# Optimization experiments

Hardware: AMD Instinct MI355X
Metric: run time of the kernel (lower is better)

## Reference

```python
import jax, jax.numpy as jnp
import numpy as np

K = 1024  # codebook size
D = 256   # embedding dim


def setup_inputs() -> dict:
    key = jax.random.key(0)
    k1, k2 = jax.random.split(key)
    z_e_x = jax.random.normal(k1, (32, D, 32, 32), dtype=jnp.float32)  # NCHW
    # nn.Embedding weight initialized uniform(-1/K, 1/K)
    W = jax.random.uniform(k2, (K, D), dtype=jnp.float32, minval=-1.0 / K, maxval=1.0 / K)
    return {"z_e_x": z_e_x, "W": W}


def reference(z_e_x, W):
    # permute NCHW -> NHWC, flatten spatial, nearest-codebook lookup (vq)
    z = jnp.transpose(z_e_x, (0, 2, 3, 1))            # [B, H, Wd, D]
    B, H, Wd, Dd = z.shape
    flat = z.reshape(-1, Dd)                           # [N, D]
    # squared L2 distances: ||z||^2 - 2 z.W^T + ||W||^2
    z_sq = jnp.sum(flat * flat, axis=1, keepdims=True)         # [N, 1]
    w_sq = jnp.sum(W * W, axis=1)                               # [K]
    dists = z_sq - 2.0 * (flat @ W.T) + w_sq[None, :]           # [N, K]
    idx = jnp.argmin(dists, axis=1)                             # [N]
    latents = idx.reshape(B, H, Wd)                             # [B, H, Wd] int indices
    return latents
```

## Files before the change

### kernel.cpp

```cpp
#include <hip/hip_runtime.h>

#define NPOS 32768
#define DDIM 256
#define KCODES 1024

typedef __attribute__((ext_vector_type(8))) short bf16x8;
typedef __attribute__((ext_vector_type(4))) float f32x4;
typedef unsigned long long u64;

__device__ __forceinline__ float sqr_rn(float x) {
    float r = x * x;
    asm volatile("" : "+v"(r));
    return r;
}
__device__ __forceinline__ float add_rn(float a, float b) {
    float r = a + b;
    asm volatile("" : "+v"(r));
    return r;
}

__device__ __forceinline__ unsigned short f2bf(float x) {
    unsigned u = __float_as_uint(x);
    return (unsigned short)((u + 0x7fffu + ((u >> 16) & 1u)) >> 16);
}

__device__ __forceinline__ u64 packm(float s, int code) {
    unsigned b = __float_as_uint(s);
    unsigned mm = ((unsigned)((int)b >> 31)) | 0x80000000u;
    return ((u64)(b ^ mm) << 32) | (unsigned)code;
}

__global__ __launch_bounds__(256) void prep(const float* __restrict__ z,
                                            const float* __restrict__ W,
                                            float* __restrict__ wsq,
                                            unsigned short* __restrict__ zb16t,
                                            unsigned short* __restrict__ wb16t) {
    __shared__ unsigned short Ls[8 * 1024];
    const int t = threadIdx.x;
    if (blockIdx.x < 1024) {
        const int img = blockIdx.x >> 5;
        const int dc  = blockIdx.x & 31;
        const int kk  = dc >> 2, kq = dc & 3;
        const float* zr = z + img * (DDIM * 1024) + dc * 8 * 1024;
#pragma unroll
        for (int e = 0; e < 8; ++e) {
            const float4 v = *(const float4*)&zr[e * 1024 + t * 4];
            unsigned short* o = &Ls[e * 1024 + t * 4];
            o[0] = f2bf(v.x); o[1] = f2bf(v.y); o[2] = f2bf(v.z); o[3] = f2bf(v.w);
        }
        __syncthreads();
#pragma unroll
        for (int j = 0; j < 4; ++j) {
            const int m = t + j * 256;
            const int mtile = img * 8 + (m >> 7);
            bf16x8 o;
#pragma unroll
            for (int e = 0; e < 8; ++e) o[e] = (short)Ls[e * 1024 + m];
            *(bf16x8*)&zb16t[mtile * 32768 + kk * 4096 + kq * 1024 + (m & 127) * 8] = o;
        }
    } else {
        const int bid = blockIdx.x - 1024;
        const int row = bid * 16 + (t >> 4);
        const int j   = t & 15;
        const float* base = W + row * DDIM + (j & 7) + (j >> 3) * 128;
        float r = sqr_rn(base[0]);
#pragma unroll
        for (int i = 1; i < 16; ++i) r = add_rn(r, sqr_rn(base[i * 8]));
#pragma unroll
        for (int m = 1; m <= 8; m <<= 1) r = add_rn(r, __shfl_xor(r, m));
        if (j == 0) wsq[row] = r;
#pragma unroll
        for (int jj = 0; jj < 2; ++jj) {
            const int u  = t + jj * 256;
            const int n  = bid * 16 + (u >> 5);
            const int k8 = u & 31;
            const float4 f0 = *(const float4*)&W[n * DDIM + k8 * 8];
            const float4 f1 = *(const float4*)&W[n * DDIM + k8 * 8 + 4];
            bf16x8 o;
            o[0] = (short)f2bf(f0.x); o[1] = (short)f2bf(f0.y);
            o[2] = (short)f2bf(f0.z); o[3] = (short)f2bf(f0.w);
            o[4] = (short)f2bf(f1.x); o[5] = (short)f2bf(f1.y);
            o[6] = (short)f2bf(f1.z); o[7] = (short)f2bf(f1.w);
            const int kk = k8 >> 2, kq = k8 & 3;
            *(bf16x8*)&wb16t[(n >> 8) * 65536 + kk * 8192 + kq * 2048 + (n & 255) * 8] = o;
        }
    }
}

__global__ __launch_bounds__(256) __attribute__((amdgpu_waves_per_eu(2, 2)))
void gemm_top2(const unsigned short* __restrict__ zb16t,
               const unsigned short* __restrict__ wb16t,
               const float* __restrict__ wsq, u64* __restrict__ cand) {
    __shared__ u64 redU[4096];

    const int t    = threadIdx.x;
    const int w    = t >> 6;
    const int l    = t & 63;
    const int ln   = l & 15;
    const int q    = l >> 4;
    const int mw   = (w & 1) * 64;
    const int nw   = (w >> 1) * 128;
    const int mblk = blockIdx.x >> 2;
    const int nblk = blockIdx.x & 3;
    const int m0   = mblk * 128;
    const int n0   = nblk * 256;

    const char* aLane = (const char*)zb16t + (size_t)mblk * 65536 + q * 2048 + (mw + ln) * 16;
    const char* bLane = (const char*)wb16t + (size_t)nblk * 131072 + q * 4096 + (nw + ln) * 16;

    f32x4 acc[4][8];
#pragma unroll
    for (int a = 0; a < 4; ++a)
#pragma unroll
        for (int b = 0; b < 8; ++b) acc[a][b] = (f32x4)(0.f);

    bf16x8 afr[4], anx[4];
#pragma unroll
    for (int mf = 0; mf < 4; ++mf)
        afr[mf] = *(const bf16x8*)(aLane + mf * 256);

#pragma unroll 1
    for (int kk = 0; kk < 8; ++kk) {
        bf16x8 bfr[8];
#pragma unroll
        for (int nf = 0; nf < 8; ++nf)
            bfr[nf] = *(const bf16x8*)(bLane + kk * 16384 + nf * 256);
        if (kk < 7) {
#pragma unroll
            for (int mf = 0; mf < 4; ++mf)
                anx[mf] = *(const bf16x8*)(aLane + (kk + 1) * 8192 + mf * 256);
        }
#pragma unroll
        for (int nf = 0; nf < 8; ++nf)
#pragma unroll
            for (int mf = 0; mf < 4; ++mf)
                acc[mf][nf] = __builtin_amdgcn_mfma_f32_16x16x32_bf16(
                    afr[mf], bfr[nf], acc[mf][nf], 0, 0, 0);
#pragma unroll
        for (int mf = 0; mf < 4; ++mf) afr[mf] = anx[mf];
    }

    float wq[8];
#pragma unroll
    for (int nf = 0; nf < 8; ++nf) wq[nf] = wsq[n0 + nw + nf * 16 + ln];

#pragma unroll
    for (int mf = 0; mf < 4; ++mf) {
#pragma unroll
        for (int reg = 0; reg < 4; ++reg) {
            const int row = mw + mf * 16 + q * 4 + reg;
            float s0 = 1e30f, s1 = 1e30f;
            int   i0 = 0,     i1 = 0;
#pragma unroll
            for (int nf = 0; nf < 8; ++nf) {
                const float s  = fmaf(-2.f, acc[mf][nf][reg], wq[nf]);
                const int   cc = n0 + nw + nf * 16 + ln;
                if (s < s0)      { s1 = s0; i1 = i0; s0 = s; i0 = cc; }
                else if (s < s1) { s1 = s; i1 = cc; }
            }
            u64 p0 = packm(s0, i0), p1 = packm(s1, i1);
            const u64 o0 = __shfl_xor(p0, 1);
            const u64 o1 = __shfl_xor(p1, 1);
            const u64 c0 = (p0 < o0) ? p0 : o0;
            const u64 hi = (p0 < o0) ? o0 : p0;
            const u64 lo = (p1 < o1) ? p1 : o1;
            const u64 c1 = (hi < lo) ? hi : lo;
            if ((ln & 1) == 0) {
                u64* slot = &redU[row * 32 + (w >> 1) * 16 + (ln >> 1) * 2];
                slot[0] = c0;
                slot[1] = c1;
            }
        }
    }
    __syncthreads();
    {
        const int r2 = t >> 1, half = t & 1;
        u64 c0 = ~0ull, c1 = ~0ull;
#pragma unroll
        for (int j = 0; j < 16; ++j) {
            const u64 v = redU[r2 * 32 + half * 16 + j];
            if (v < c0)      { c1 = c0; c0 = v; }
            else if (v < c1) { c1 = v; }
        }
        __syncthreads();
        redU[r2 * 4 + half * 2]     = c0;
        redU[r2 * 4 + half * 2 + 1] = c1;
    }
    __syncthreads();
    if (t < 128) {
        const u64 a = redU[t * 4], b = redU[t * 4 + 1];
        const u64 c = redU[t * 4 + 2], d = redU[t * 4 + 3];
        const u64 m1 = (a < c) ? a : c;
        const u64 hi = (a < c) ? c : a;
        const u64 lo = (b < d) ? b : d;
        const u64 m2 = (hi < lo) ? hi : lo;
        u64* o = &cand[(u64)(m0 + t) * 8 + nblk * 2];
        o[0] = m1;
        o[1] = m2;
    }
}

#define ZS 260
__global__ __launch_bounds__(256) void rescore(const float* __restrict__ z,
                                               const float* __restrict__ W,
                                               const float* __restrict__ wsq,
                                               const u64* __restrict__ cand,
                                               int* __restrict__ out) {
    __shared__ float Zs[32 * ZS];
    const int t  = threadIdx.x;
    const int m0 = blockIdx.x * 32;
    const float* zimg = z + (m0 >> 10) * (DDIM * 1024) + (m0 & 1023);
#pragma unroll
    for (int j = 0; j < 8; ++j) {
        const int f4 = t + j * 256;
        const int d = f4 >> 3, p4 = f4 & 7;
        const float4 v = *(const float4*)&zimg[d * 1024 + p4 * 4];
        Zs[(p4 * 4 + 0) * ZS + d] = v.x;
        Zs[(p4 * 4 + 1) * ZS + d] = v.y;
        Zs[(p4 * 4 + 2) * ZS + d] = v.z;
        Zs[(p4 * 4 + 3) * ZS + d] = v.w;
    }
    __syncthreads();
    const int pl = t >> 3, slot = t & 7;
    const int p = m0 + pl;
    const float* zr = &Zs[pl * ZS];

    float h0 = sqr_rn(zr[slot]);
    float h1 = sqr_rn(zr[128 + slot]);
#pragma unroll
    for (int i = 1; i < 16; ++i) {
        h0 = add_rn(h0, sqr_rn(zr[slot + 8 * i]));
        h1 = add_rn(h1, sqr_rn(zr[128 + slot + 8 * i]));
    }
#pragma unroll
    for (int m = 1; m <= 4; m <<= 1) {
        h0 = add_rn(h0, __shfl_xor(h0, m));
        h1 = add_rn(h1, __shfl_xor(h1, m));
    }
    const float zq = add_rn(h0, h1);

    const int code = (int)(unsigned)(cand[(u64)p * 8 + slot] & 0xffffffffULL);
    const float* wr = W + code * DDIM;
    float M = 0.f;
#pragma unroll 8
    for (int d4 = 0; d4 < 64; ++d4) {
        const float4 zv = *(const float4*)&zr[d4 * 4];
        const float4 wv = *(const float4*)&wr[d4 * 4];
        M = fmaf(zv.x, wv.x, M);
        M = fmaf(zv.y, wv.y, M);
        M = fmaf(zv.z, wv.z, M);
        M = fmaf(zv.w, wv.w, M);
    }
    const float s = add_rn(fmaf(-2.f, M, zq), wsq[code]);
    u64 v = ((u64)__float_as_uint(s) << 32) | (unsigned)code;
#pragma unroll
    for (int m = 1; m <= 4; m <<= 1) {
        const u64 o = __shfl_xor(v, m);
        if (o < v) v = o;
    }
    if (slot == 0) out[p] = (int)(unsigned)(v & 0xffffffffULL);
}

extern "C" void kernel_launch(void* const* d_in, const int* in_sizes, int n_in,
                              void* d_out, int out_size, void* d_ws, size_t ws_size,
                              hipStream_t stream) {
    const float* z = (const float*)d_in[0];
    const float* W = (const float*)d_in[1];
    int* out = (int*)d_out;

    char* ws = (char*)d_ws;
    float*          wsq   = (float*)ws;
    u64*            cand  = (u64*)(ws + 4096);
    unsigned short* zb16t = (unsigned short*)(ws + 2101248);
    unsigned short* wb16t = (unsigned short*)(ws + 18878464);

    prep<<<1024 + KCODES / 16, 256, 0, stream>>>(z, W, wsq, zb16t, wb16t);
    gemm_top2<<<(NPOS / 128) * 4, 256, 0, stream>>>(zb16t, wb16t, wsq, cand);
    rescore<<<NPOS / 32, 256, 0, stream>>>(z, W, wsq, cand, out);
}
```

Measured before the change: 144.4 us.

## Fuse z conversion, bf16 GEMM top-2 and fp32 rescore into one kernel

Replaces the three-kernel pipeline with a W-only prep kernel and a single fused kernel. Each block converts a 64-position tile of z to bf16 in shared memory, loops over all four codebook blocks with MFMA to keep per-row top-2 candidates in LDS, then rescores the candidates in fp32 from a reloaded z tile. This removes the global round trips for the bf16 z copy and the candidate array, plus one launch. In exchange, W bf16 fragments are streamed from global memory by each of the 512 blocks, the M tile shrinks to 64, and the phases inside a block run serially with extra barriers.

```diff
diff --git a/kernel.cpp b/kernel.cpp
--- a/kernel.cpp
+++ b/kernel.cpp
@@ -30,235 +30,219 @@
     return ((u64)(b ^ mm) << 32) | (unsigned)code;
 }
 
-__global__ __launch_bounds__(256) void prep(const float* __restrict__ z,
-                                            const float* __restrict__ W,
-                                            float* __restrict__ wsq,
-                                            unsigned short* __restrict__ zb16t,
-                                            unsigned short* __restrict__ wb16t) {
-    __shared__ unsigned short Ls[8 * 1024];
-    const int t = threadIdx.x;
-    if (blockIdx.x < 1024) {
-        const int img = blockIdx.x >> 5;
-        const int dc  = blockIdx.x & 31;
-        const int kk  = dc >> 2, kq = dc & 3;
-        const float* zr = z + img * (DDIM * 1024) + dc * 8 * 1024;
-#pragma unroll
-        for (int e = 0; e < 8; ++e) {
-            const float4 v = *(const float4*)&zr[e * 1024 + t * 4];
-            unsigned short* o = &Ls[e * 1024 + t * 4];
-            o[0] = f2bf(v.x); o[1] = f2bf(v.y); o[2] = f2bf(v.z); o[3] = f2bf(v.w);
-        }
-        __syncthreads();
-#pragma unroll
-        for (int j = 0; j < 4; ++j) {
-            const int m = t + j * 256;
-            const int mtile = img * 8 + (m >> 7);
+__global__ __launch_bounds__(256) void wprep(const float* __restrict__ W,
+                                             float* __restrict__ wsq,
+                                             unsigned short* __restrict__ wb16t) {
+    const int t   = threadIdx.x;
+    const int bid = blockIdx.x;
+    const int row = bid * 16 + (t >> 4);
+    const int j   = t & 15;
+    const float* base = W + row * DDIM + (j & 7) + (j >> 3) * 128;
+    float r = sqr_rn(base[0]);
+#pragma unroll
+    for (int i = 1; i < 16; ++i) r = add_rn(r, sqr_rn(base[i * 8]));
+#pragma unroll
+    for (int m = 1; m <= 8; m <<= 1) r = add_rn(r, __shfl_xor(r, m));
+    if (j == 0) wsq[row] = r;
+#pragma unroll
+    for (int jj = 0; jj < 2; ++jj) {
+        const int u  = t + jj * 256;
+        const int n  = bid * 16 + (u >> 5);
+        const int k8 = u & 31;
+        const float4 f0 = *(const float4*)&W[n * DDIM + k8 * 8];
+        const float4 f1 = *(const float4*)&W[n * DDIM + k8 * 8 + 4];
+        bf16x8 o;
+        o[0] = (short)f2bf(f0.x); o[1] = (short)f2bf(f0.y);
+        o[2] = (short)f2bf(f0.z); o[3] = (short)f2bf(f0.w);
+        o[4] = (short)f2bf(f1.x); o[5] = (short)f2bf(f1.y);
+        o[6] = (short)f2bf(f1.z); o[7] = (short)f2bf(f1.w);
+        const int kk = k8 >> 2, kq = k8 & 3;
+        *(bf16x8*)&wb16t[(n >> 8) * 65536 + kk * 8192 + kq * 2048 + (n & 255) * 8] = o;
+    }
+}
+
+#define ZS 260
+__global__ __launch_bounds__(256) __attribute__((amdgpu_waves_per_eu(2, 2)))
+void vq_fused(const float* __restrict__ z,
+              const float* __restrict__ W,
+              const float* __restrict__ wsq,
+              const unsigned short* __restrict__ wb16t,
+              int* __restrict__ out) {
+    union Sm {
+        unsigned short At[16384];
+        float          Zs[32 * ZS];
+    };
+    __shared__ Sm  sm;
+    __shared__ u64 redL[64 * 8];
+    __shared__ u64 candL[64 * 8];
+
+    const int t   = threadIdx.x;
+    const int bid = blockIdx.x;
+    const int img = bid >> 4;
+    const int p0  = (bid & 15) * 64;
+
+    {
+        const float* zbase = z + img * (DDIM * 1024) + p0;
+#pragma unroll
+        for (int jj = 0; jj < 8; ++jj) {
+            const int u_ = t + jj * 256;
+            const int m  = u_ & 63;
+            const int k8 = u_ >> 6;
+            const float* src = zbase + k8 * 8192 + m;
             bf16x8 o;
 #pragma unroll
-            for (int e = 0; e < 8; ++e) o[e] = (short)Ls[e * 1024 + m];
-            *(bf16x8*)&zb16t[mtile * 32768 + kk * 4096 + kq * 1024 + (m & 127) * 8] = o;
-        }
-    } else {
-        const int bid = blockIdx.x - 1024;
-        const int row = bid * 16 + (t >> 4);
-        const int j   = t & 15;
-        const float* base = W + row * DDIM + (j & 7) + (j >> 3) * 128;
-        float r = sqr_rn(base[0]);
-#pragma unroll
-        for (int i = 1; i < 16; ++i) r = add_rn(r, sqr_rn(base[i * 8]));
-#pragma unroll
-        for (int m = 1; m <= 8; m <<= 1) r = add_rn(r, __shfl_xor(r, m));
-        if (j == 0) wsq[row] = r;
-#pragma unroll
-        for (int jj = 0; jj < 2; ++jj) {
-            const int u  = t + jj * 256;
-            const int n  = bid * 16 + (u >> 5);
-            const int k8 = u & 31;
-            const float4 f0 = *(const float4*)&W[n * DDIM + k8 * 8];
-            const float4 f1 = *(const float4*)&W[n * DDIM + k8 * 8 + 4];
-            bf16x8 o;
-            o[0] = (short)f2bf(f0.x); o[1] = (short)f2bf(f0.y);
-            o[2] = (short)f2bf(f0.z); o[3] = (short)f2bf(f0.w);
-            o[4] = (short)f2bf(f1.x); o[5] = (short)f2bf(f1.y);
-            o[6] = (short)f2bf(f1.z); o[7] = (short)f2bf(f1.w);
-            const int kk = k8 >> 2, kq = k8 & 3;
-            *(bf16x8*)&wb16t[(n >> 8) * 65536 + kk * 8192 + kq * 2048 + (n & 255) * 8] = o;
-        }
-    }
-}
-
-__global__ __launch_bounds__(256) __attribute__((amdgpu_waves_per_eu(2, 2)))
-void gemm_top2(const unsigned short* __restrict__ zb16t,
-               const unsigned short* __restrict__ wb16t,
-               const float* __restrict__ wsq, u64* __restrict__ cand) {
-    __shared__ u64 redU[4096];
-
-    const int t    = threadIdx.x;
-    const int w    = t >> 6;
-    const int l    = t & 63;
-    const int ln   = l & 15;
-    const int q    = l >> 4;
-    const int mw   = (w & 1) * 64;
-    const int nw   = (w >> 1) * 128;
-    const int mblk = blockIdx.x >> 2;
-    const int nblk = blockIdx.x & 3;
-    const int m0   = mblk * 128;
-    const int n0   = nblk * 256;
-
-    const char* aLane = (const char*)zb16t + (size_t)mblk * 65536 + q * 2048 + (mw + ln) * 16;
-    const char* bLane = (const char*)wb16t + (size_t)nblk * 131072 + q * 4096 + (nw + ln) * 16;
-
-    f32x4 acc[4][8];
-#pragma unroll
-    for (int a = 0; a < 4; ++a)
-#pragma unroll
-        for (int b = 0; b < 8; ++b) acc[a][b] = (f32x4)(0.f);
-
-    bf16x8 afr[4], anx[4];
-#pragma unroll
-    for (int mf = 0; mf < 4; ++mf)
-        afr[mf] = *(const bf16x8*)(aLane + mf * 256);
+            for (int e = 0; e < 8; ++e) o[e] = (short)f2bf(src[e * 1024]);
+            *(bf16x8*)&sm.At[k8 * 512 + m * 8] = o;
+        }
+    }
+    __syncthreads();
+
+    const int w  = t >> 6;
+    const int l  = t & 63;
+    const int ln = l & 15;
+    const int q  = l >> 4;
+    const int nw = w * 64;
+
+    const char* aBase = (const char*)sm.At + q * 1024 + ln * 16;
+    const char* bBase = (const char*)wb16t + q * 4096 + (nw + ln) * 16;
 
 #pragma unroll 1
-    for (int kk = 0; kk < 8; ++kk) {
-        bf16x8 bfr[8];
-#pragma unroll
-        for (int nf = 0; nf < 8; ++nf)
-            bfr[nf] = *(const bf16x8*)(bLane + kk * 16384 + nf * 256);
-        if (kk < 7) {
+    for (int nblk = 0; nblk < 4; ++nblk) {
+        const int n0 = nblk * 256;
+        float wq[4];
+#pragma unroll
+        for (int nf = 0; nf < 4; ++nf) wq[nf] = wsq[n0 + nw + nf * 16 + ln];
+
+        f32x4 acc[4][4];
+#pragma unroll
+        for (int a = 0; a < 4; ++a)
+#pragma unroll
+            for (int b = 0; b < 4; ++b) acc[a][b] = (f32x4)(0.f);
+
+        const char* bP = bBase + nblk * 131072;
+        bf16x8 bfr[4], bnx[4];
+#pragma unroll
+        for (int nf = 0; nf < 4; ++nf) bfr[nf] = *(const bf16x8*)(bP + nf * 256);
+
+#pragma unroll 1
+        for (int kk = 0; kk < 8; ++kk) {
+            if (kk < 7) {
+#pragma unroll
+                for (int nf = 0; nf < 4; ++nf)
+                    bnx[nf] = *(const bf16x8*)(bP + (kk + 1) * 16384 + nf * 256);
+            }
+            bf16x8 afr[4];
 #pragma unroll
             for (int mf = 0; mf < 4; ++mf)
-                anx[mf] = *(const bf16x8*)(aLane + (kk + 1) * 8192 + mf * 256);
-        }
-#pragma unroll
-        for (int nf = 0; nf < 8; ++nf)
-#pragma unroll
-            for (int mf = 0; mf < 4; ++mf)
-                acc[mf][nf] = __builtin_amdgcn_mfma_f32_16x16x32_bf16(
-                    afr[mf], bfr[nf], acc[mf][nf], 0, 0, 0);
-#pragma unroll
-        for (int mf = 0; mf < 4; ++mf) afr[mf] = anx[mf];
-    }
-
-    float wq[8];
-#pragma unroll
-    for (int nf = 0; nf < 8; ++nf) wq[nf] = wsq[n0 + nw + nf * 16 + ln];
-
-#pragma unroll
-    for (int mf = 0; mf < 4; ++mf) {
-#pragma unroll
-        for (int reg = 0; reg < 4; ++reg) {
-            const int row = mw + mf * 16 + q * 4 + reg;
-            float s0 = 1e30f, s1 = 1e30f;
-            int   i0 = 0,     i1 = 0;
-#pragma unroll
-            for (int nf = 0; nf < 8; ++nf) {
-                const float s  = fmaf(-2.f, acc[mf][nf][reg], wq[nf]);
-                const int   cc = n0 + nw + nf * 16 + ln;
-                if (s < s0)      { s1 = s0; i1 = i0; s0 = s; i0 = cc; }
-                else if (s < s1) { s1 = s; i1 = cc; }
+                afr[mf] = *(const bf16x8*)(aBase + kk * 4096 + mf * 256);
+#pragma unroll
+            for (int nf = 0; nf < 4; ++nf)
+#pragma unroll
+                for (int mf = 0; mf < 4; ++mf)
+                    acc[mf][nf] = __builtin_amdgcn_mfma_f32_16x16x32_bf16(
+                        afr[mf], bfr[nf], acc[mf][nf], 0, 0, 0);
+#pragma unroll
+            for (int nf = 0; nf < 4; ++nf) bfr[nf] = bnx[nf];
+        }
+
+#pragma unroll
+        for (int mf = 0; mf < 4; ++mf) {
+#pragma unroll
+            for (int reg = 0; reg < 4; ++reg) {
+                const int row = mf * 16 + q * 4 + reg;
+                float s0 = 1e30f, s1 = 1e30f;
+                int   i0 = 0,     i1 = 0;
+#pragma unroll
+                for (int nf = 0; nf < 4; ++nf) {
+                    const float s  = fmaf(-2.f, acc[mf][nf][reg], wq[nf]);
+                    const int   cc = n0 + nw + nf * 16 + ln;
+                    if (s < s0)      { s1 = s0; i1 = i0; s0 = s; i0 = cc; }
+                    else if (s < s1) { s1 = s; i1 = cc; }
+                }
+                u64 c0 = packm(s0, i0), c1 = packm(s1, i1);
+#pragma unroll
+                for (int m = 1; m <= 8; m <<= 1) {
+                    const u64 o0 = __shfl_xor(c0, m);
+                    const u64 o1 = __shfl_xor(c1, m);
+                    const u64 hi = (c0 < o0) ? o0 : c0;
+                    c0 = (c0 < o0) ? c0 : o0;
+                    const u64 lo = (c1 < o1) ? c1 : o1;
+                    c1 = (hi < lo) ? hi : lo;
+                }
+                if (ln == 0) {
+                    redL[row * 8 + w * 2]     = c0;
+                    redL[row * 8 + w * 2 + 1] = c1;
+                }
             }
-            u64 p0 = packm(s0, i0), p1 = packm(s1, i1);
-            const u64 o0 = __shfl_xor(p0, 1);
-            const u64 o1 = __shfl_xor(p1, 1);
-            const u64 c0 = (p0 < o0) ? p0 : o0;
-            const u64 hi = (p0 < o0) ? o0 : p0;
-            const u64 lo = (p1 < o1) ? p1 : o1;
-            const u64 c1 = (hi < lo) ? hi : lo;
-            if ((ln & 1) == 0) {
-                u64* slot = &redU[row * 32 + (w >> 1) * 16 + (ln >> 1) * 2];
-                slot[0] = c0;
-                slot[1] = c1;
+        }
+        __syncthreads();
+        if (t < 64) {
+            u64 c0 = ~0ull, c1 = ~0ull;
+#pragma unroll
+            for (int jj = 0; jj < 8; ++jj) {
+                const u64 v = redL[t * 8 + jj];
+                if (v < c0)      { c1 = c0; c0 = v; }
+                else if (v < c1) { c1 = v; }
             }
-        }
-    }
-    __syncthreads();
-    {
-        const int r2 = t >> 1, half = t & 1;
-        u64 c0 = ~0ull, c1 = ~0ull;
-#pragma unroll
-        for (int j = 0; j < 16; ++j) {
-            const u64 v = redU[r2 * 32 + half * 16 + j];
-            if (v < c0)      { c1 = c0; c0 = v; }
-            else if (v < c1) { c1 = v; }
-        }
-        __syncthreads();
-        redU[r2 * 4 + half * 2]     = c0;
-        redU[r2 * 4 + half * 2 + 1] = c1;
-    }
-    __syncthreads();
-    if (t < 128) {
-        const u64 a = redU[t * 4], b = redU[t * 4 + 1];
-        const u64 c = redU[t * 4 + 2], d = redU[t * 4 + 3];
-        const u64 m1 = (a < c) ? a : c;
-        const u64 hi = (a < c) ? c : a;
-        const u64 lo = (b < d) ? b : d;
-        const u64 m2 = (hi < lo) ? hi : lo;
-        u64* o = &cand[(u64)(m0 + t) * 8 + nblk * 2];
-        o[0] = m1;
-        o[1] = m2;
-    }
-}
-
-#define ZS 260
-__global__ __launch_bounds__(256) void rescore(const float* __restrict__ z,
-                                               const float* __restrict__ W,
-                                               const float* __restrict__ wsq,
-                                               const u64* __restrict__ cand,
-                                               int* __restrict__ out) {
-    __shared__ float Zs[32 * ZS];
-    const int t  = threadIdx.x;
-    const int m0 = blockIdx.x * 32;
-    const float* zimg = z + (m0 >> 10) * (DDIM * 1024) + (m0 & 1023);
-#pragma unroll
-    for (int j = 0; j < 8; ++j) {
-        const int f4 = t + j * 256;
-        const int d = f4 >> 3, p4 = f4 & 7;
-        const float4 v = *(const float4*)&zimg[d * 1024 + p4 * 4];
-        Zs[(p4 * 4 + 0) * ZS + d] = v.x;
-        Zs[(p4 * 4 + 1) * ZS + d] = v.y;
-        Zs[(p4 * 4 + 2) * ZS + d] = v.z;
-        Zs[(p4 * 4 + 3) * ZS + d] = v.w;
-    }
-    __syncthreads();
-    const int pl = t >> 3, slot = t & 7;
-    const int p = m0 + pl;
-    const float* zr = &Zs[pl * ZS];
-
-    float h0 = sqr_rn(zr[slot]);
-    float h1 = sqr_rn(zr[128 + slot]);
-#pragma unroll
-    for (int i = 1; i < 16; ++i) {
-        h0 = add_rn(h0, sqr_rn(zr[slot + 8 * i]));
-        h1 = add_rn(h1, sqr_rn(zr[128 + slot + 8 * i]));
-    }
-#pragma unroll
-    for (int m = 1; m <= 4; m <<= 1) {
-        h0 = add_rn(h0, __shfl_xor(h0, m));
-        h1 = add_rn(h1, __shfl_xor(h1, m));
-    }
-    const float zq = add_rn(h0, h1);
-
-    const int code = (int)(unsigned)(cand[(u64)p * 8 + slot] & 0xffffffffULL);
-    const float* wr = W + code * DDIM;
-    float M = 0.f;
+            candL[t * 8 + nblk * 2]     = c0;
+            candL[t * 8 + nblk * 2 + 1] = c1;
+        }
+        __syncthreads();
+    }
+
+    const float* zimg = z + img * (DDIM * 1024) + p0;
+#pragma unroll 1
+    for (int c = 0; c < 2; ++c) {
+#pragma unroll
+        for (int jj = 0; jj < 8; ++jj) {
+            const int f4 = t + jj * 256;
+            const int d = f4 >> 3, p4 = f4 & 7;
+            const float4 v = *(const float4*)&zimg[d * 1024 + c * 32 + p4 * 4];
+            sm.Zs[(p4 * 4 + 0) * ZS + d] = v.x;
+            sm.Zs[(p4 * 4 + 1) * ZS + d] = v.y;
+            sm.Zs[(p4 * 4 + 2) * ZS + d] = v.z;
+            sm.Zs[(p4 * 4 + 3) * ZS + d] = v.w;
+        }
+        __syncthreads();
+        const int pl = t >> 3, slot = t & 7;
+        const float* zr = &sm.Zs[pl * ZS];
+
+        float h0 = sqr_rn(zr[slot]);
+        float h1 = sqr_rn(zr[128 + slot]);
+#pragma unroll
+        for (int i = 1; i < 16; ++i) {
+            h0 = add_rn(h0, sqr_rn(zr[slot + 8 * i]));
+            h1 = add_rn(h1, sqr_rn(zr[128 + slot + 8 * i]));
+        }
+#pragma unroll
+        for (int m = 1; m <= 4; m <<= 1) {
+            h0 = add_rn(h0, __shfl_xor(h0, m));
+            h1 = add_rn(h1, __shfl_xor(h1, m));
+        }
+        const float zq = add_rn(h0, h1);
+
+        const int code = (int)(unsigned)(candL[(c * 32 + pl) * 8 + slot] & 0xffffffffULL);
+        const float* wr = W + code * DDIM;
+        float M = 0.f;
 #pragma unroll 8
-    for (int d4 = 0; d4 < 64; ++d4) {
-        const float4 zv = *(const float4*)&zr[d4 * 4];
-        const float4 wv = *(const float4*)&wr[d4 * 4];
-        M = fmaf(zv.x, wv.x, M);
-        M = fmaf(zv.y, wv.y, M);
-        M = fmaf(zv.z, wv.z, M);
-        M = fmaf(zv.w, wv.w, M);
-    }
-    const float s = add_rn(fmaf(-2.f, M, zq), wsq[code]);
-    u64 v = ((u64)__float_as_uint(s) << 32) | (unsigned)code;
-#pragma unroll
-    for (int m = 1; m <= 4; m <<= 1) {
-        const u64 o = __shfl_xor(v, m);
-        if (o < v) v = o;
-    }
-    if (slot == 0) out[p] = (int)(unsigned)(v & 0xffffffffULL);
+        for (int d4 = 0; d4 < 64; ++d4) {
+            const float4 zv = *(const float4*)&zr[d4 * 4];
+            const float4 wv = *(const float4*)&wr[d4 * 4];
+            M = fmaf(zv.x, wv.x, M);
+            M = fmaf(zv.y, wv.y, M);
+            M = fmaf(zv.z, wv.z, M);
+            M = fmaf(zv.w, wv.w, M);
+        }
+        const float s = add_rn(fmaf(-2.f, M, zq), wsq[code]);
+        u64 v = ((u64)__float_as_uint(s) << 32) | (unsigned)code;
+#pragma unroll
+        for (int m = 1; m <= 4; m <<= 1) {
+            const u64 o = __shfl_xor(v, m);
+            if (o < v) v = o;
+        }
+        if (slot == 0) out[img * 1024 + p0 + c * 32 + pl] = (int)(unsigned)(v & 0xffffffffULL);
+        __syncthreads();
+    }
 }
 
 extern "C" void kernel_launch(void* const* d_in, const int* in_sizes, int n_in,
@@ -270,11 +254,8 @@
 
     char* ws = (char*)d_ws;
     float*          wsq   = (float*)ws;
-    u64*            cand  = (u64*)(ws + 4096);
-    unsigned short* zb16t = (unsigned short*)(ws + 2101248);
-    unsigned short* wb16t = (unsigned short*)(ws + 18878464);
-
-    prep<<<1024 + KCODES / 16, 256, 0, stream>>>(z, W, wsq, zb16t, wb16t);
-    gemm_top2<<<(NPOS / 128) * 4, 256, 0, stream>>>(zb16t, wb16t, wsq, cand);
-    rescore<<<NPOS / 32, 256, 0, stream>>>(z, W, wsq, cand, out);
-}
+    unsigned short* wb16t = (unsigned short*)(ws + 4096);
+
+    wprep<<<KCODES / 16, 256, 0, stream>>>(W, wsq, wb16t);
+    vq_fused<<<NPOS / 64, 256, 0, stream>>>(z, W, wsq, wb16t, out);
+}
```

Result: slower. 152.4 us (+5.5%).
